# Kernel optimization log

Measured on AMD Instinct MI355X. Metric: run time of the kernel, lower is better.

The kernel has to match this reference:

```python
import jax, jax.numpy as jnp
import numpy as np
from jax.ops import segment_sum

N_NODES = 100000
N_EDGES = 1250000
F_IN = 64
F_OUT = 64


def setup_inputs() -> dict:
    key = jax.random.key(0)
    k1, k2, k3, k4, k5 = jax.random.split(key, 5)
    x = jax.random.normal(k1, (N_NODES, F_IN), dtype=jnp.float32)
    edge_index = jax.random.randint(k2, (2, N_EDGES), 0, N_NODES, dtype=jnp.int32)
    edge_weight = jax.random.uniform(k3, (2, N_EDGES, 1), dtype=jnp.float32)
    # glorot_uniform for Dense kernels [in, out]
    lim = float(np.sqrt(6.0 / (F_IN + F_OUT)))
    W_src = jax.random.uniform(k4, (F_IN, F_OUT), minval=-lim, maxval=lim, dtype=jnp.float32)
    W_dst = jax.random.uniform(k5, (F_IN, F_OUT), minval=-lim, maxval=lim, dtype=jnp.float32)
    b_src = jnp.zeros((F_OUT,), dtype=jnp.float32)
    b_dst = jnp.zeros((F_OUT,), dtype=jnp.float32)
    return {"x": x, "edge_index": edge_index, "edge_weight": edge_weight,
            "W_src": W_src, "W_dst": W_dst, "b_src": b_src, "b_dst": b_dst}


def reference(x, edge_index, edge_weight, W_src, W_dst, b_src, b_dst):
    num_nodes = x.shape[0]
    senders, receivers = edge_index[0], edge_index[1]
    ew_s2d, ew_d2s = edge_weight[0], edge_weight[1]  # [E, 1] each
    x_gather = x[senders]  # [E, F_IN]
    agg_s2d = segment_sum(x_gather * ew_s2d, receivers, num_segments=num_nodes)
    agg_d2s = segment_sum(x_gather * ew_d2s, receivers, num_segments=num_nodes)
    out_s2d = agg_s2d @ W_src + b_src
    out_d2s = agg_d2s @ W_dst + b_dst
    return (out_s2d, out_d2s)
```

## Files before the change

### kernel.cpp

```cpp
#include <hip/hip_runtime.h>
#include <hip/hip_fp16.h>

#define N_NODES 100000
#define N_EDGES 1250000
#define F 64
#define SCAN_CHUNK 1024
#define NBLK_SCAN ((N_NODES + SCAN_CHUNK - 1) / SCAN_CHUNK)
#define NPB 16
#define TP 18


__global__ __launch_bounds__(256) void hist_kernel(const int* __restrict__ ei,
                                                   int* __restrict__ counts,
                                                   int* __restrict__ rank) {
    int e = blockIdx.x * 256 + threadIdx.x;
    if (e < N_EDGES) rank[e] = atomicAdd(&counts[ei[N_EDGES + e]], 1);
}

__global__ __launch_bounds__(256) void scan_reduce_kernel(const int* __restrict__ counts,
                                                          int* __restrict__ partials) {
    int base = blockIdx.x * SCAN_CHUNK + threadIdx.x * 4;
    int s = 0;
    if (base + 3 < N_NODES) {
        int4 c = *(const int4*)&counts[base];
        s = c.x + c.y + c.z + c.w;
    }
    for (int d = 32; d > 0; d >>= 1) s += __shfl_down(s, d);
    __shared__ int lds[4];
    int lane = threadIdx.x & 63, wave = threadIdx.x >> 6;
    if (lane == 0) lds[wave] = s;
    __syncthreads();
    if (threadIdx.x == 0) partials[blockIdx.x] = lds[0] + lds[1] + lds[2] + lds[3];
}

__global__ __launch_bounds__(256) void scan_apply_kernel(const int* __restrict__ counts,
                                                         const int* __restrict__ partials,
                                                         int* __restrict__ off) {
    __shared__ int sh_red[4];
    __shared__ int sh_base;
    __shared__ int wsum[4];
    int t = threadIdx.x;
    int lane = t & 63, wave = t >> 6;

    int pp = 0;
    if (t < blockIdx.x && t < NBLK_SCAN) pp = partials[t];
    for (int d = 32; d > 0; d >>= 1) pp += __shfl_down(pp, d);
    if (lane == 0) sh_red[wave] = pp;
    __syncthreads();
    if (t == 0) sh_base = sh_red[0] + sh_red[1] + sh_red[2] + sh_red[3];

    int base = blockIdx.x * SCAN_CHUNK + t * 4;
    int4 c = {0, 0, 0, 0};
    bool act = (base + 3 < N_NODES);
    if (act) c = *(const int4*)&counts[base];
    int s = c.x + c.y + c.z + c.w;

    int xs = s;
    for (int d = 1; d < 64; d <<= 1) {
        int y = __shfl_up(xs, d);
        if (lane >= d) xs += y;
    }
    if (lane == 63) wsum[wave] = xs;
    __syncthreads();
    int pre = xs - s;
    for (int w = 0; w < wave; ++w) pre += wsum[w];
    pre += sh_base;

    if (act) {
        int o0 = pre, o1 = o0 + c.x, o2 = o1 + c.y, o3 = o2 + c.z;
        int4 o = {o0, o1, o2, o3};
        *(int4*)&off[base] = o;
        if (base + 4 == N_NODES) off[N_NODES] = o3 + c.w;
    }
}

__global__ __launch_bounds__(256) void permute_kernel(const int* __restrict__ ei,
                                                      const float* __restrict__ ew,
                                                      const int* __restrict__ off,
                                                      const int* __restrict__ rank,
                                                      int2* __restrict__ pay) {
    int e = blockIdx.x * 256 + threadIdx.x;
    if (e >= N_EDGES) return;
    int r = ei[N_EDGES + e];
    int pos = off[r] + rank[e];
    __half2 h = __floats2half2_rn(ew[e], ew[N_EDGES + e]);
    int2 p;
    p.x = ei[e];
    p.y = *(const int*)&h;
    pay[pos] = p;
}

__global__ __launch_bounds__(256, 8) void agg_gemm_kernel(
    const float* __restrict__ x, const int* __restrict__ off,
    const int2* __restrict__ pay,
    const float* __restrict__ Wsrc, const float* __restrict__ Wdst,
    const float* __restrict__ bsrc, const float* __restrict__ bdst,
    float* __restrict__ outA, float* __restrict__ outB)
{
    __shared__ float tA[F * TP];
    __shared__ float tB[F * TP];
    int t = threadIdx.x;
    int w = t >> 6;
    int lane = t & 63;
    int g = lane >> 4;
    int l4 = lane & 15;
    int nIB = w * 4 + g;
    int n = blockIdx.x * NPB + nIB;

    const float4* x4 = (const float4*)x;
    int beg = off[n];
    int end = off[n + 1];

    float4 accA = {0.f, 0.f, 0.f, 0.f};
    float4 accB = {0.f, 0.f, 0.f, 0.f};

    if (beg < end) {
        int last = end - 1;
        int2 p0 = pay[beg];
        float4 x0 = x4[(size_t)p0.x * 16 + l4];
        int i1 = min(beg + 1, last);
        int2 p1 = pay[i1];
        float4 x1 = x4[(size_t)p1.x * 16 + l4];
        for (int i = beg; i < end; ++i) {
            int i2 = min(i + 2, last);
            int2 p2 = pay[i2];
            float4 x2 = x4[(size_t)p2.x * 16 + l4];
            float2 wv = __half22float2(*(const __half2*)&p0.y);
            accA.x += x0.x * wv.x; accA.y += x0.y * wv.x;
            accA.z += x0.z * wv.x; accA.w += x0.w * wv.x;
            accB.x += x0.x * wv.y; accB.y += x0.y * wv.y;
            accB.z += x0.z * wv.y; accB.w += x0.w * wv.y;
            p0 = p1; x0 = x1;
            p1 = p2; x1 = x2;
        }
    }

    #pragma unroll
    for (int c = 0; c < 4; ++c) {
        tA[(4 * l4 + c) * TP + nIB] = ((const float*)&accA)[c];
        tB[(4 * l4 + c) * TP + nIB] = ((const float*)&accB)[c];
    }

    __syncthreads();

    int dir = t >> 7;
    int tx = t & 15;
    int ty = (t >> 4) & 7;
    const float* W    = dir ? Wdst : Wsrc;
    const float* bias = dir ? bdst : bsrc;
    const float* tile = dir ? tB : tA;
    float* out        = dir ? outB : outA;
    int j4 = tx * 4, n2 = ty * 2;

    float4 bj = *(const float4*)&bias[j4];
    float4 a0 = bj, a1 = bj;
    #pragma unroll 8
    for (int k = 0; k < F; ++k) {
        float4 wv = *(const float4*)&W[k * F + j4];
        float2 v  = *(const float2*)&tile[k * TP + n2];
        a0.x += v.x * wv.x; a0.y += v.x * wv.y; a0.z += v.x * wv.z; a0.w += v.x * wv.w;
        a1.x += v.y * wv.x; a1.y += v.y * wv.y; a1.z += v.y * wv.z; a1.w += v.y * wv.w;
    }
    int nb = blockIdx.x * NPB + n2;
    *(float4*)&out[(size_t)(nb + 0) * F + j4] = a0;
    *(float4*)&out[(size_t)(nb + 1) * F + j4] = a1;
}


__global__ __launch_bounds__(256) void scatter_fallback(const float4* __restrict__ x4,
                                                        const int* __restrict__ ei,
                                                        const float* __restrict__ ew,
                                                        float* __restrict__ aggA,
                                                        float* __restrict__ aggB) {
    int t = blockIdx.x * blockDim.x + threadIdx.x;
    int e = t >> 4;
    int lane16 = t & 15;
    if (e >= N_EDGES) return;
    int src = ei[e], dst = ei[N_EDGES + e];
    float w0 = ew[e], w1 = ew[N_EDGES + e];
    float4 v = x4[(size_t)src * 16 + lane16];
    int base = dst * F + lane16 * 4;
    atomicAdd(&aggA[base + 0], v.x * w0); atomicAdd(&aggA[base + 1], v.y * w0);
    atomicAdd(&aggA[base + 2], v.z * w0); atomicAdd(&aggA[base + 3], v.w * w0);
    atomicAdd(&aggB[base + 0], v.x * w1); atomicAdd(&aggB[base + 1], v.y * w1);
    atomicAdd(&aggB[base + 2], v.z * w1); atomicAdd(&aggB[base + 3], v.w * w1);
}

__global__ __launch_bounds__(256) void matmul_fallback(float* __restrict__ outA, float* __restrict__ outB,
                                                       const float* __restrict__ Wsrc, const float* __restrict__ Wdst,
                                                       const float* __restrict__ bsrc, const float* __restrict__ bdst) {
    __shared__ float lWs[F * F];
    __shared__ float lWd[F * F];
    for (int i = threadIdx.x; i < F * F / 4; i += blockDim.x) {
        ((float4*)lWs)[i] = ((const float4*)Wsrc)[i];
        ((float4*)lWd)[i] = ((const float4*)Wdst)[i];
    }
    __syncthreads();
    int wave = (blockIdx.x * blockDim.x + threadIdx.x) >> 6;
    int lane = threadIdx.x & 63;
    if (wave >= N_NODES) return;
    size_t rowbase = (size_t)wave * F;
    float a0 = outA[rowbase + lane], a1 = outB[rowbase + lane];
    float acc0 = bsrc[lane], acc1 = bdst[lane];
    #pragma unroll
    for (int k = 0; k < F; ++k) {
        acc0 += __shfl(a0, k) * lWs[k * F + lane];
        acc1 += __shfl(a1, k) * lWd[k * F + lane];
    }
    outA[rowbase + lane] = acc0;
    outB[rowbase + lane] = acc1;
}


extern "C" void kernel_launch(void* const* d_in, const int* in_sizes, int n_in,
                              void* d_out, int out_size, void* d_ws, size_t ws_size,
                              hipStream_t stream) {
    const float* x    = (const float*)d_in[0];
    const int*   ei   = (const int*)d_in[1];
    const float* ew   = (const float*)d_in[2];
    const float* Wsrc = (const float*)d_in[3];
    const float* Wdst = (const float*)d_in[4];
    const float* bsrc = (const float*)d_in[5];
    const float* bdst = (const float*)d_in[6];

    float* outA = (float*)d_out;
    float* outB = (float*)d_out + (size_t)N_NODES * F;

    const size_t OFF_COUNTS   = 0;
    const size_t OFF_OFF      = 400128;
    const size_t OFF_PARTIALS = 800640;
    const size_t OFF_RANK     = 801152;
    const size_t OFF_PAY      = 5801152;
    const size_t REQ          = 15801152;

    if (ws_size >= REQ) {
        char* ws = (char*)d_ws;
        int*  counts   = (int*)(ws + OFF_COUNTS);
        int*  off      = (int*)(ws + OFF_OFF);
        int*  partials = (int*)(ws + OFF_PARTIALS);
        int*  rank     = (int*)(ws + OFF_RANK);
        int2* pay      = (int2*)(ws + OFF_PAY);

        hipMemsetAsync(counts, 0, (size_t)N_NODES * sizeof(int), stream);

        int eblk = (N_EDGES + 255) / 256;
        hist_kernel<<<eblk, 256, 0, stream>>>(ei, counts, rank);
        scan_reduce_kernel<<<NBLK_SCAN, 256, 0, stream>>>(counts, partials);
        scan_apply_kernel<<<NBLK_SCAN, 256, 0, stream>>>(counts, partials, off);
        permute_kernel<<<eblk, 256, 0, stream>>>(ei, ew, off, rank, pay);
        agg_gemm_kernel<<<N_NODES / NPB, 256, 0, stream>>>(
            x, off, pay, Wsrc, Wdst, bsrc, bdst, outA, outB);
    } else {
        hipMemsetAsync(d_out, 0, (size_t)out_size * sizeof(float), stream);
        int blocks_scatter = (N_EDGES * 16 + 255) / 256;
        scatter_fallback<<<blocks_scatter, 256, 0, stream>>>((const float4*)x, ei, ew, outA, outB);
        int blocks_mm = (N_NODES * 64 + 255) / 256;
        matmul_fallback<<<blocks_mm, 256, 0, stream>>>(outA, outB, Wsrc, Wdst, bsrc, bdst);
    }
}
```

Before: 255.9 us.

## Gather fp16 copy of node features with deeper 4-edge prefetch pipeline

Adds a kernel that converts x to fp16 into the workspace, reusing the counts/rank region after permute is done. The aggregation kernel then gathers 8-byte half rows instead of 16-byte float rows, halving gather traffic. The edge loop is unrolled by four with an eight-deep prefetch of payload and feature loads, and the tail is masked by zeroing weights. This costs an extra conversion pass, more registers (occupancy hint lowered from 8 to 6), and fp16 rounding of inputs, which reduces accuracy.

```diff
diff --git a/kernel.cpp b/kernel.cpp
--- a/kernel.cpp
+++ b/kernel.cpp
@@ -90,8 +90,23 @@
     pay[pos] = p;
 }
 
-__global__ __launch_bounds__(256, 8) void agg_gemm_kernel(
-    const float* __restrict__ x, const int* __restrict__ off,
+__global__ __launch_bounds__(256) void cvt_kernel(const float* __restrict__ x,
+                                                  __half* __restrict__ xh) {
+    int i = blockIdx.x * 256 + threadIdx.x;
+    int base = i * 4;
+    if (base < N_NODES * F) {
+        float4 v = *(const float4*)&x[base];
+        __half2 h0 = __floats2half2_rn(v.x, v.y);
+        __half2 h1 = __floats2half2_rn(v.z, v.w);
+        uint2 u;
+        u.x = *(const unsigned int*)&h0;
+        u.y = *(const unsigned int*)&h1;
+        *(uint2*)&xh[base] = u;
+    }
+}
+
+__global__ __launch_bounds__(256, 6) void agg_gemm_kernel(
+    const __half* __restrict__ xh, const int* __restrict__ off,
     const int2* __restrict__ pay,
     const float* __restrict__ Wsrc, const float* __restrict__ Wdst,
     const float* __restrict__ bsrc, const float* __restrict__ bdst,
@@ -107,7 +122,6 @@
     int nIB = w * 4 + g;
     int n = blockIdx.x * NPB + nIB;
 
-    const float4* x4 = (const float4*)x;
     int beg = off[n];
     int end = off[n + 1];
 
@@ -116,22 +130,48 @@
 
     if (beg < end) {
         int last = end - 1;
-        int2 p0 = pay[beg];
-        float4 x0 = x4[(size_t)p0.x * 16 + l4];
-        int i1 = min(beg + 1, last);
-        int2 p1 = pay[i1];
-        float4 x1 = x4[(size_t)p1.x * 16 + l4];
-        for (int i = beg; i < end; ++i) {
-            int i2 = min(i + 2, last);
-            int2 p2 = pay[i2];
-            float4 x2 = x4[(size_t)p2.x * 16 + l4];
-            float2 wv = __half22float2(*(const __half2*)&p0.y);
-            accA.x += x0.x * wv.x; accA.y += x0.y * wv.x;
-            accA.z += x0.z * wv.x; accA.w += x0.w * wv.x;
-            accB.x += x0.x * wv.y; accB.y += x0.y * wv.y;
-            accB.z += x0.z * wv.y; accB.w += x0.w * wv.y;
-            p0 = p1; x0 = x1;
-            p1 = p2; x1 = x2;
+        int2 pa0 = pay[beg];
+        int2 pa1 = pay[min(beg + 1, last)];
+        int2 pa2 = pay[min(beg + 2, last)];
+        int2 pa3 = pay[min(beg + 3, last)];
+        int2 pb0 = pay[min(beg + 4, last)];
+        int2 pb1 = pay[min(beg + 5, last)];
+        int2 pb2 = pay[min(beg + 6, last)];
+        int2 pb3 = pay[min(beg + 7, last)];
+        uint2 xa0 = *(const uint2*)(xh + (size_t)pa0.x * F + l4 * 4);
+        uint2 xa1 = *(const uint2*)(xh + (size_t)pa1.x * F + l4 * 4);
+        uint2 xa2 = *(const uint2*)(xh + (size_t)pa2.x * F + l4 * 4);
+        uint2 xa3 = *(const uint2*)(xh + (size_t)pa3.x * F + l4 * 4);
+
+        for (int i = beg; i < end; i += 4) {
+            int2 pc0 = pay[min(i + 8, last)];
+            int2 pc1 = pay[min(i + 9, last)];
+            int2 pc2 = pay[min(i + 10, last)];
+            int2 pc3 = pay[min(i + 11, last)];
+            uint2 xb0 = *(const uint2*)(xh + (size_t)pb0.x * F + l4 * 4);
+            uint2 xb1 = *(const uint2*)(xh + (size_t)pb1.x * F + l4 * 4);
+            uint2 xb2 = *(const uint2*)(xh + (size_t)pb2.x * F + l4 * 4);
+            uint2 xb3 = *(const uint2*)(xh + (size_t)pb3.x * F + l4 * 4);
+
+#define EDGE(J, PJ, XJ)                                                   \
+            {                                                             \
+                float2 wv = __half22float2(*(const __half2*)&PJ.y);       \
+                if (i + J >= end) { wv.x = 0.f; wv.y = 0.f; }             \
+                float2 lo = __half22float2(*(const __half2*)&XJ.x);       \
+                float2 hi = __half22float2(*(const __half2*)&XJ.y);       \
+                accA.x += lo.x * wv.x; accA.y += lo.y * wv.x;             \
+                accA.z += hi.x * wv.x; accA.w += hi.y * wv.x;             \
+                accB.x += lo.x * wv.y; accB.y += lo.y * wv.y;             \
+                accB.z += hi.x * wv.y; accB.w += hi.y * wv.y;             \
+            }
+            EDGE(0, pa0, xa0)
+            EDGE(1, pa1, xa1)
+            EDGE(2, pa2, xa2)
+            EDGE(3, pa3, xa3)
+#undef EDGE
+            pa0 = pb0; pa1 = pb1; pa2 = pb2; pa3 = pb3;
+            pb0 = pc0; pb1 = pc1; pb2 = pc2; pb3 = pc3;
+            xa0 = xb0; xa1 = xb1; xa2 = xb2; xa3 = xb3;
         }
     }
 
@@ -226,20 +266,22 @@
     float* outA = (float*)d_out;
     float* outB = (float*)d_out + (size_t)N_NODES * F;
 
+    const size_t OFF_XH       = 0;
     const size_t OFF_COUNTS   = 0;
-    const size_t OFF_OFF      = 400128;
-    const size_t OFF_PARTIALS = 800640;
-    const size_t OFF_RANK     = 801152;
-    const size_t OFF_PAY      = 5801152;
-    const size_t REQ          = 15801152;
+    const size_t OFF_PARTIALS = 400128;
+    const size_t OFF_RANK     = 400640;
+    const size_t OFF_OFF      = 12800256;
+    const size_t OFF_PAY      = 13200768;
+    const size_t REQ          = 23200768;
 
     if (ws_size >= REQ) {
         char* ws = (char*)d_ws;
-        int*  counts   = (int*)(ws + OFF_COUNTS);
-        int*  off      = (int*)(ws + OFF_OFF);
-        int*  partials = (int*)(ws + OFF_PARTIALS);
-        int*  rank     = (int*)(ws + OFF_RANK);
-        int2* pay      = (int2*)(ws + OFF_PAY);
+        int*    counts   = (int*)(ws + OFF_COUNTS);
+        int*    partials = (int*)(ws + OFF_PARTIALS);
+        int*    rank     = (int*)(ws + OFF_RANK);
+        int*    off      = (int*)(ws + OFF_OFF);
+        int2*   pay      = (int2*)(ws + OFF_PAY);
+        __half* xh       = (__half*)(ws + OFF_XH);
 
         hipMemsetAsync(counts, 0, (size_t)N_NODES * sizeof(int), stream);
 
@@ -248,8 +290,10 @@
         scan_reduce_kernel<<<NBLK_SCAN, 256, 0, stream>>>(counts, partials);
         scan_apply_kernel<<<NBLK_SCAN, 256, 0, stream>>>(counts, partials, off);
         permute_kernel<<<eblk, 256, 0, stream>>>(ei, ew, off, rank, pay);
+        int cblk = (N_NODES * F / 4 + 255) / 256;
+        cvt_kernel<<<cblk, 256, 0, stream>>>(x, xh);
         agg_gemm_kernel<<<N_NODES / NPB, 256, 0, stream>>>(
-            x, off, pay, Wsrc, Wdst, bsrc, bdst, outA, outB);
+            xh, off, pay, Wsrc, Wdst, bsrc, bdst, outA, outB);
     } else {
         hipMemsetAsync(d_out, 0, (size_t)out_size * sizeof(float), stream);
         int blocks_scatter = (N_EDGES * 16 + 255) / 256;
```

Result: slower. 262.6 us (+2.6%).
